# Performance work log

Hardware: AMD Instinct MI355X
Metric: run time of the kernel (lower is better)

## Reference

```python
import jax, jax.numpy as jnp
import numpy as np

B, L, D = 2, 2048, 1024
H = 16
C = 128            # chunk_size
N = L // C         # num chunks
SCALE = float(np.sqrt(D))  # softmax_scale = sqrt(d_model)


def setup_inputs() -> dict:
    key = jax.random.key(0)
    ks = jax.random.split(key, 5)
    return {
        "x": jax.random.normal(ks[0], (B, L, D), dtype=jnp.float32),
        "w_qkv": jax.random.normal(ks[1], (D, 3 * D), dtype=jnp.float32) * (1.0 / np.sqrt(D)),
        "b_qkv": jax.random.normal(ks[2], (3 * D,), dtype=jnp.float32) * 0.02,
        "w_o": jax.random.normal(ks[3], (D, D), dtype=jnp.float32) * (1.0 / np.sqrt(D)),
        "b_o": jax.random.normal(ks[4], (D,), dtype=jnp.float32) * 0.02,
    }


def reference(x, w_qkv, b_qkv, w_o, b_o):
    b, l, d = x.shape
    hd = d // H
    qkv = x @ w_qkv + b_qkv                         # (B,L,3D)
    q, k, v = jnp.split(qkv, 3, axis=-1)
    q = q.reshape(b, l, H, hd)
    k = k.reshape(b, l, H, hd)
    v = v.reshape(b, l, H, hd)

    q_chunks = q.reshape(b, N, C, H, hd)
    k_chunks = k.reshape(b, N, C, H, hd)
    # mean_pool over the chunk dim
    q_pool = q_chunks.mean(axis=2)                  # (B,N,H,hd)
    k_pool = k_chunks.mean(axis=2)

    token2chunk = jnp.einsum('blhd,bnhd->bhln', q, k_pool)          # (B,H,L,N)
    chunk2token = jnp.einsum('bnhd,bnchd->bhnc', q_pool, k_chunks)  # (B,H,N,C)
    # outer product over (n,c) -> full (B,H,L,L) score matrix
    A = token2chunk[..., :, None] * chunk2token[:, :, None, :, :]   # (B,H,L,N,C)
    A = A.reshape(b, H, l, l)

    # direct intra-chunk attention overwrites the diagonal blocks
    direct = jnp.einsum('bnqhd,bnkhd->bhnqk', q_chunks, k_chunks)   # (B,H,N,C,C)
    A6 = A.reshape(b, H, N, C, N, C)
    eye = jnp.eye(N, dtype=bool)[:, None, :, None]                  # (N,1,N,1)
    A6 = jnp.where(eye, direct[:, :, :, :, None, :], A6)
    A = A6.reshape(b, H, l, l)

    # causal mask applied multiplicatively (masked scores become 0, NOT -inf)
    causal = jnp.tril(jnp.ones((l, l), dtype=bool))
    A = jnp.where(causal, A, 0.0) / SCALE
    A = jax.nn.softmax(A, axis=-1)

    out = jnp.einsum('bhqv,bvhd->bhqd', A, v)       # (B,H,L,hd)
    out = out.transpose(0, 2, 1, 3).reshape(b, l, d)
    return out @ w_o + b_o
```

## Files before the change

### kernel.cpp

```cpp
#include <hip/hip_runtime.h>
#include <math.h>

#define B_   2
#define L_   2048
#define D_   1024
#define H_   16
#define HD_  64
#define C_   128
#define N_   16
#define INV_SCALE 0.03125f
#define SCL2 0.0450842200f

typedef _Float16 h8 __attribute__((ext_vector_type(8)));
typedef _Float16 h4 __attribute__((ext_vector_type(4)));
typedef float    f4 __attribute__((ext_vector_type(4)));

#define MFMA16(a, b, c) __builtin_amdgcn_mfma_f32_16x16x32_f16((a), (b), (c), 0, 0, 0)

#if __has_builtin(__builtin_amdgcn_exp2f)
#define EXP2(x) __builtin_amdgcn_exp2f(x)
#else
#define EXP2(x) exp2f(x)
#endif

__device__ __forceinline__ void gl_lds16(const void* g, void* l) {
  __builtin_amdgcn_global_load_lds(
      (const __attribute__((address_space(1))) void*)g,
      (__attribute__((address_space(3))) void*)l, 16, 0, 0);
}

#define SBAR()  do { __builtin_amdgcn_sched_barrier(0); \
                     __builtin_amdgcn_s_barrier();      \
                     __builtin_amdgcn_sched_barrier(0); } while (0)
#define LGKM0() do { asm volatile("s_waitcnt lgkmcnt(0)" ::: "memory"); \
                     __builtin_amdgcn_sched_barrier(0); } while (0)
#define VMW(n)  do { asm volatile("s_waitcnt vmcnt(" #n ")" ::: "memory"); \
                     __builtin_amdgcn_sched_barrier(0); } while (0)

__global__ __launch_bounds__(256) void prep_kernel(
    const float* __restrict__ X, _Float16* __restrict__ Xh,
    const float* __restrict__ Wq, _Float16* __restrict__ WqT,
    const float* __restrict__ Wo, _Float16* __restrict__ WoT)
{
  __shared__ float ts[32][36];
  const int tid = threadIdx.x;
  const int id = blockIdx.x;
  if (id < 4096) {
    int i = id * 1024 + tid * 4;
    float4 v = *(const float4*)(X + i);
    h4 o = { (_Float16)v.x, (_Float16)v.y, (_Float16)v.z, (_Float16)v.w };
    *(h4*)(Xh + i) = o;
    return;
  }
  const float* W; _Float16* WT; int Nc, bx, by;
  if (id < 7168) {
    int idx = id - 4096;
    W = Wq; WT = WqT; Nc = 3072; bx = idx % 96; by = idx / 96;
  } else {
    int idx = id - 7168;
    W = Wo; WT = WoT; Nc = 1024; bx = idx & 31; by = idx >> 5;
  }
  const int n0 = bx * 32, k0 = by * 32;
  {
    int kr = tid >> 3, nc4 = (tid & 7) * 4;
    float4 v = *(const float4*)&W[(size_t)(k0 + kr) * Nc + n0 + nc4];
    ts[kr][nc4+0] = v.x; ts[kr][nc4+1] = v.y; ts[kr][nc4+2] = v.z; ts[kr][nc4+3] = v.w;
  }
  __syncthreads();
  {
    int nr = tid >> 3, kc4 = (tid & 7) * 4;
    h4 o = { (_Float16)ts[kc4+0][nr], (_Float16)ts[kc4+1][nr],
             (_Float16)ts[kc4+2][nr], (_Float16)ts[kc4+3][nr] };
    *(h4*)&WT[(size_t)(n0 + nr) * 1024 + k0 + kc4] = o;
  }
}

__global__ __launch_bounds__(512, 2) void qkv256_kernel(
    const _Float16* __restrict__ A, const _Float16* __restrict__ Bt,
    const float* __restrict__ bias,
    _Float16* __restrict__ Qh, _Float16* __restrict__ Kh, _Float16* __restrict__ VT,
    float* __restrict__ QP, float* __restrict__ KP, float* __restrict__ VCS)
{
  __shared__ __align__(16) _Float16 As[2][16384];
  __shared__ __align__(16) _Float16 Bs[2][12288];

  const int tid = threadIdx.x;
  const int w = tid >> 6, lane = tid & 63;
  const int q = lane >> 4, r = lane & 15, r7 = r & 7;
  const int wm = w >> 2, wn = w & 3;

  const int id = blockIdx.x, xcd = id & 7, slot = id >> 3;
  const int m0 = ((xcd >> 1) * 4 + (slot & 3)) * 256;
  const int n0 = ((xcd & 1) * 8 + (slot >> 2)) * 192;

  const int srow = tid >> 3;
  const int spart = (tid & 7) ^ (srow & 7);
  const _Float16* Asrc = A  + (size_t)(m0 + srow) * 1024 + spart * 8;
  const _Float16* Bsrc = Bt + (size_t)(n0 + srow) * 1024 + spart * 8;
  const int ldst = w * 512;

  const int aoffb = (wm * 128 + r) * 64;
  const int boffb = (wn * 48 + r) * 64;
  const int k0s = (q ^ r7) << 3;
  const int k1s = ((4 + q) ^ r7) << 3;

  auto stA = [&](int cc, int ko, int qq) {
    gl_lds16(Asrc + (size_t)qq * 65536 + ko, &As[cc][qq * 4096 + ldst]);
  };
  auto stB = [&](int cc, int ko, int qq) {
    gl_lds16(Bsrc + (size_t)qq * 65536 + ko, &Bs[cc][qq * 4096 + ldst]);
  };

  f4 acc[8][3];
  #pragma unroll
  for (int m = 0; m < 8; ++m)
    #pragma unroll
    for (int n = 0; n < 3; ++n) acc[m][n] = (f4){0.f, 0.f, 0.f, 0.f};

  stB(0, 0, 0); stB(0, 0, 1); stB(0, 0, 2);
  stA(0, 0, 0); stA(0, 0, 2); stA(0, 0, 1); stA(0, 0, 3);
  VMW(2);
  SBAR();

  for (int t = 0; t < 16; ++t) {
    const int c = t & 1;
    const _Float16* __restrict__ Ab = As[c];
    const _Float16* __restrict__ Bb = Bs[c];
    const int kt = (t + 1) << 6;
    const bool pf = (t < 15);
    h8 af[4], bf[3];

    #pragma unroll
    for (int m = 0; m < 4; ++m) af[m] = *(const h8*)&Ab[aoffb + m * 1024 + k0s];
    #pragma unroll
    for (int n = 0; n < 3; ++n) bf[n] = *(const h8*)&Bb[boffb + n * 1024 + k0s];
    if (pf) { stB(c ^ 1, kt, 0); stB(c ^ 1, kt, 1); }
    SBAR();
    LGKM0();
    __builtin_amdgcn_s_setprio(1);
    #pragma unroll
    for (int m = 0; m < 4; ++m)
      #pragma unroll
      for (int n = 0; n < 3; ++n) acc[m][n] = MFMA16(af[m], bf[n], acc[m][n]);
    __builtin_amdgcn_s_setprio(0);
    __builtin_amdgcn_sched_barrier(0);
    if (pf) { VMW(2); } else { VMW(0); }
    SBAR();

    #pragma unroll
    for (int m = 0; m < 4; ++m) af[m] = *(const h8*)&Ab[aoffb + (4 + m) * 1024 + k0s];
    if (pf) { stB(c ^ 1, kt, 2); stA(c ^ 1, kt, 0); }
    SBAR();
    LGKM0();
    __builtin_amdgcn_s_setprio(1);
    #pragma unroll
    for (int m = 0; m < 4; ++m)
      #pragma unroll
      for (int n = 0; n < 3; ++n) acc[4 + m][n] = MFMA16(af[m], bf[n], acc[4 + m][n]);
    __builtin_amdgcn_s_setprio(0);
    __builtin_amdgcn_sched_barrier(0);
    SBAR();

    #pragma unroll
    for (int m = 0; m < 4; ++m) af[m] = *(const h8*)&Ab[aoffb + m * 1024 + k1s];
    #pragma unroll
    for (int n = 0; n < 3; ++n) bf[n] = *(const h8*)&Bb[boffb + n * 1024 + k1s];
    if (pf) { stA(c ^ 1, kt, 2); stA(c ^ 1, kt, 1); }
    SBAR();
    LGKM0();
    __builtin_amdgcn_s_setprio(1);
    #pragma unroll
    for (int m = 0; m < 4; ++m)
      #pragma unroll
      for (int n = 0; n < 3; ++n) acc[m][n] = MFMA16(af[m], bf[n], acc[m][n]);
    __builtin_amdgcn_s_setprio(0);
    __builtin_amdgcn_sched_barrier(0);
    SBAR();

    #pragma unroll
    for (int m = 0; m < 4; ++m) af[m] = *(const h8*)&Ab[aoffb + (4 + m) * 1024 + k1s];
    if (pf) {
      stA(c ^ 1, kt, 3);
      VMW(2);
    }
    SBAR();
    LGKM0();
    __builtin_amdgcn_s_setprio(1);
    #pragma unroll
    for (int m = 0; m < 4; ++m)
      #pragma unroll
      for (int n = 0; n < 3; ++n) acc[4 + m][n] = MFMA16(af[m], bf[n], acc[4 + m][n]);
    __builtin_amdgcn_s_setprio(0);
    __builtin_amdgcn_sched_barrier(0);
    SBAR();
  }

  const int rb = m0 + wm * 128;
  const int b2 = rb >> 11;
  const int nch = (rb & 2047) >> 7;
  #pragma unroll
  for (int tc = 0; tc < 3; ++tc) {
    const int gn = n0 + wn * 48 + tc * 16 + r;
    const float bj = bias[gn];
    const int which = gn >> 10, rem = gn & 1023;
    const int h2 = rem >> 6, d2 = rem & 63;
    if (which < 2) {
      _Float16* dst = which == 0 ? Qh : Kh;
      #pragma unroll
      for (int m = 0; m < 8; ++m)
        #pragma unroll
        for (int i = 0; i < 4; ++i) {
          const int gm = rb + m * 16 + q * 4 + i;
          const int l2 = gm & 2047;
          dst[(((size_t)(b2 * H_ + h2)) * L_ + l2) * HD_ + d2] =
              (_Float16)(acc[m][tc][i] + bj);
        }
    } else {
      #pragma unroll
      for (int m = 0; m < 8; ++m) {
        const int gm0 = rb + m * 16 + q * 4;
        const int l2 = gm0 & 2047;
        h4 hv = { (_Float16)(acc[m][tc][0] + bj), (_Float16)(acc[m][tc][1] + bj),
                  (_Float16)(acc[m][tc][2] + bj), (_Float16)(acc[m][tc][3] + bj) };
        *(h4*)&VT[((size_t)(b2 * H_ + h2) * HD_ + d2) * L_ + l2] = hv;
      }
    }
    float s2 = 0.f;
    #pragma unroll
    for (int m = 0; m < 8; ++m)
      #pragma unroll
      for (int i = 0; i < 4; ++i) s2 += acc[m][tc][i];
    s2 += __shfl_xor(s2, 16);
    s2 += __shfl_xor(s2, 32);
    if (q == 0) {
      const size_t o = (((size_t)(b2 * H_ + h2)) * N_ + nch) * HD_ + d2;
      if (which == 0)      QP[o] = s2 * (1.f / 128.f) + bj;
      else if (which == 1) KP[o] = s2 * (1.f / 128.f) + bj;
      else                 VCS[o] = s2 + 128.f * bj;
    }
  }
}

template<int MT>
__global__ __launch_bounds__(256, 4) void gemm16_kernel(
    const _Float16* __restrict__ A, const _Float16* __restrict__ Bt,
    const float* __restrict__ bias,
    _Float16* __restrict__ Qh, _Float16* __restrict__ Kh, _Float16* __restrict__ VT,
    float* __restrict__ out,
    float* __restrict__ QP, float* __restrict__ KP, float* __restrict__ VCS,
    int Kd, int mode)
{
  constexpr int SM = MT / 32;
  __shared__ __align__(16) _Float16 As[2][MT * 32];
  __shared__ __align__(16) _Float16 Bs[2][4096];
  __shared__ float cred[2][128];
  const int tid = threadIdx.x;
  const int lane = tid & 63, w = tid >> 6;
  const int q = lane >> 4, r = lane & 15;
  const int mb = (w >> 1) * (MT / 2);
  const int nb = (w & 1) * 64;

  int m0, n0;
  {
    const int id = blockIdx.x;
    const int xcd = id & 7, slot = id >> 3;
    if constexpr (MT == 128) {
      n0 = (xcd * 3 + (slot % 3)) * 128;
      m0 = (slot / 3) * 128;
    } else {
      m0 = (xcd * 8 + (slot >> 3)) * 64;
      n0 = (slot & 7) * 128;
    }
  }

  const int Rr = tid >> 2;
  const int cd = (tid & 3) ^ ((Rr >> 1) & 3);
  const _Float16* Ag = A + (size_t)(m0 + Rr) * Kd + cd * 8;
  const _Float16* Bg = Bt + (size_t)(n0 + Rr) * Kd + cd * 8;
  const size_t rowStep = (size_t)64 * Kd;

  f4 acc[SM][4];
  #pragma unroll
  for (int s = 0; s < SM; ++s)
    #pragma unroll
    for (int t = 0; t < 4; ++t) acc[s][t] = (f4){0.f, 0.f, 0.f, 0.f};

  const int nIter = Kd >> 5;
  const int koff = (q ^ ((r >> 1) & 3)) << 3;

  auto stage = [&](int bf, int kt) {
    _Float16* Asl = &As[bf][w * 512];
    _Float16* Bsl = &Bs[bf][w * 512];
    gl_lds16(Ag + kt, Asl);
    if constexpr (MT == 128) gl_lds16(Ag + kt + rowStep, Asl + 2048);
    gl_lds16(Bg + kt, Bsl);
    gl_lds16(Bg + kt + rowStep, Bsl + 2048);
  };

  stage(0, 0);

  for (int it = 0; it < nIter; ++it) {
    __syncthreads();
    if (it + 1 < nIter) stage((it + 1) & 1, (it + 1) << 5);
    const _Float16* Ab = As[it & 1];
    const _Float16* Bb = Bs[it & 1];
    h8 af[SM], bf4[4];
    #pragma unroll
    for (int s = 0; s < SM; ++s)
      af[s] = *(const h8*)&Ab[(mb + s * 16 + r) * 32 + koff];
    #pragma unroll
    for (int t = 0; t < 4; ++t)
      bf4[t] = *(const h8*)&Bb[(nb + t * 16 + r) * 32 + koff];
    #pragma unroll
    for (int s = 0; s < SM; ++s)
      #pragma unroll
      for (int t = 0; t < 4; ++t)
        acc[s][t] = MFMA16(af[s], bf4[t], acc[s][t]);
  }

  if (mode == 0) {
    #pragma unroll
    for (int t = 0; t < 4; ++t) {
      int gn = n0 + nb + t * 16 + r;
      float bj = bias[gn];
      int which = gn >> 10, rem = gn & 1023;
      int h2 = rem >> 6, d2 = rem & 63;
      if (which < 2) {
        _Float16* dst = which == 0 ? Qh : Kh;
        #pragma unroll
        for (int s = 0; s < SM; ++s)
          #pragma unroll
          for (int i = 0; i < 4; ++i) {
            int gm = m0 + mb + s * 16 + q * 4 + i;
            int b2 = gm >> 11, l2 = gm & 2047;
            dst[(((size_t)(b2 * H_ + h2)) * L_ + l2) * HD_ + d2] =
                (_Float16)(acc[s][t][i] + bj);
          }
      } else {
        #pragma unroll
        for (int s = 0; s < SM; ++s) {
          int gm0 = m0 + mb + s * 16 + q * 4;
          int b2 = gm0 >> 11, l2 = gm0 & 2047;
          h4 hv = { (_Float16)(acc[s][t][0] + bj), (_Float16)(acc[s][t][1] + bj),
                    (_Float16)(acc[s][t][2] + bj), (_Float16)(acc[s][t][3] + bj) };
          *(h4*)&VT[((size_t)(b2 * H_ + h2) * HD_ + d2) * L_ + l2] = hv;
        }
      }
    }
    float colsum[4];
    #pragma unroll
    for (int t = 0; t < 4; ++t) {
      float s2 = 0.f;
      #pragma unroll
      for (int s = 0; s < SM; ++s)
        #pragma unroll
        for (int i = 0; i < 4; ++i) s2 += acc[s][t][i];
      s2 += __shfl_xor(s2, 16);
      s2 += __shfl_xor(s2, 32);
      colsum[t] = s2;
    }
    if (q == 0) {
      #pragma unroll
      for (int t = 0; t < 4; ++t)
        cred[w >> 1][nb + t * 16 + r] = colsum[t];
    }
    __syncthreads();
    if (tid < 128) {
      int jj = tid;
      float ssum = cred[0][jj] + cred[1][jj];
      int gn = n0 + jj;
      float bj = bias[gn];
      int which = gn >> 10, rem = gn & 1023;
      int h2 = rem >> 6, d2 = rem & 63;
      int b2 = m0 >> 11, nch = (m0 & 2047) >> 7;
      size_t o = (((size_t)(b2 * H_ + h2)) * N_ + nch) * HD_ + d2;
      if (which == 0)      QP[o] = ssum * (1.f / 128.f) + bj;
      else if (which == 1) KP[o] = ssum * (1.f / 128.f) + bj;
      else                 VCS[o] = ssum + 128.f * bj;
    }
  } else {
    #pragma unroll
    for (int t = 0; t < 4; ++t) {
      int gn = n0 + nb + t * 16 + r;
      float bj = bias[gn];
      #pragma unroll
      for (int s = 0; s < SM; ++s)
        #pragma unroll
        for (int i = 0; i < 4; ++i) {
          int gm = m0 + mb + s * 16 + q * 4 + i;
          out[(size_t)gm * 1024 + gn] = acc[s][t][i] + bj;
        }
    }
  }
}

__global__ __launch_bounds__(128) void pool2_kernel(
    const float* __restrict__ QP, const _Float16* __restrict__ Kh,
    const float* __restrict__ VCS,
    float* __restrict__ C2T, float* __restrict__ C2TMX, float* __restrict__ C2TMN,
    float* __restrict__ CSUF)
{
  __shared__ float qp_s[64];
  __shared__ float red[4];
  if (blockIdx.x >= 512) {
    int bh = blockIdx.x - 512, d = threadIdx.x;
    if (d < 64) {
      float run = 0.f;
      for (int n = N_ - 1; n >= 0; --n) {
        size_t o = ((size_t)bh * N_ + n) * HD_ + d;
        CSUF[o] = run;
        run += VCS[o];
      }
    }
    return;
  }
  int bh = blockIdx.x >> 4, n = blockIdx.x & 15, tid = threadIdx.x;
  int w = tid >> 6, lane = tid & 63;
  if (tid < 64) qp_s[tid] = QP[((size_t)bh * N_ + n) * HD_ + tid];
  const _Float16* kr = Kh + (((size_t)bh * L_) + n * C_ + tid) * HD_;
  h8 kv[8];
  #pragma unroll
  for (int c8 = 0; c8 < 8; ++c8) kv[c8] = *(const h8*)(kr + c8 * 8);
  __syncthreads();
  float s = 0.f;
  #pragma unroll
  for (int c8 = 0; c8 < 8; ++c8)
    #pragma unroll
    for (int j = 0; j < 8; ++j)
      s = fmaf((float)kv[c8][j], qp_s[c8 * 8 + j], s);
  C2T[((size_t)bh * N_ + n) * C_ + tid] = s;
  float mx = s, mn = s;
  #pragma unroll
  for (int st = 1; st <= 32; st <<= 1) {
    mx = fmaxf(mx, __shfl_xor(mx, st));
    mn = fminf(mn, __shfl_xor(mn, st));
  }
  if (lane == 0) { red[w * 2] = mx; red[w * 2 + 1] = mn; }
  __syncthreads();
  if (tid == 0) {
    C2TMX[bh * N_ + n] = fmaxf(red[0], red[2]);
    C2TMN[bh * N_ + n] = fminf(red[1], red[3]);
  }
}

__global__ __launch_bounds__(512, 4) void attn4_kernel(
    const _Float16* __restrict__ Qh, const _Float16* __restrict__ Kh,
    const _Float16* __restrict__ VT,
    const float* __restrict__ C2T, const float* __restrict__ C2TMX,
    const float* __restrict__ C2TMN, const float* __restrict__ CSUF,
    const float* __restrict__ KP, _Float16* __restrict__ AOh)
{
  __shared__ __align__(16) _Float16 buf0[8192];
  __shared__ __align__(16) _Float16 buf1[8192];
  __shared__ __align__(16) _Float16 buf2[8192];
  __shared__ __align__(16) _Float16 kp_s[1024];
  __shared__ __align__(16) float c2t_s[2][128];

  const int tid = threadIdx.x;
  const int w = tid >> 6, lane = tid & 63;
  const int q = lane >> 4, r = lane & 15;
  const int r7 = r & 7;
  const int id = blockIdx.x;
  const int bh = ((id & 7) << 2) + ((id >> 3) & 3);
  const int nq = 15 - (id >> 5);
  const int l0 = nq * 128;
  const int rowA = l0 + w * 16 + r;
  const int pcw = w * 16 + r;
  const size_t bhL = (size_t)bh * L_;
  const int b2 = bh >> 4, h2 = bh & 15;

  auto stageV = [&](_Float16* buf, int n) {
    #pragma unroll
    for (int j2 = 0; j2 < 2; ++j2) {
      int f = j2 * 512 + tid;
      int d = f >> 4, p = f & 15;
      int c16 = p ^ (d & 7);
      gl_lds16(VT + ((size_t)bh * HD_ + d) * L_ + n * C_ + c16 * 8,
               buf + (size_t)(j2 * 512 + w * 64) * 8);
    }
  };
  auto stageK = [&](_Float16* buf, int n) {
    #pragma unroll
    for (int j2 = 0; j2 < 2; ++j2) {
      int f = j2 * 512 + tid;
      int c = f >> 3, p = f & 7;
      int ck = p ^ (c & 7);
      gl_lds16(Kh + (bhL + n * C_ + c) * HD_ + ck * 8,
               buf + (size_t)(j2 * 512 + w * 64) * 8);
    }
  };
  auto stageC = [&](int bf, int n) {
    if (tid < 32)
      gl_lds16(C2T + ((size_t)bh * N_ + n) * C_ + tid * 4, &c2t_s[bf][0]);
  };

  if (tid < 256) {
    int n4 = tid >> 4, d4 = (tid & 15) * 4;
    float4 kpv = *(const float4*)&KP[((size_t)bh * N_ + n4) * HD_ + d4];
    int sd = ((((d4 >> 3) ^ (n4 & 7)) << 3) | (d4 & 7));
    h4 hv = { (_Float16)kpv.x, (_Float16)kpv.y, (_Float16)kpv.z, (_Float16)kpv.w };
    *(h4*)&kp_s[n4 * 64 + sd] = hv;
  }
  h8 qa0 = *(const h8*)(Qh + (bhL + rowA) * HD_ + q * 8);
  h8 qa1 = *(const h8*)(Qh + (bhL + rowA) * HD_ + 32 + q * 8);
  float mxL = C2TMX[bh * N_ + r];
  float mnL = C2TMN[bh * N_ + r];
  stageK(buf0, nq);
  stageV(buf2, nq);
  if (nq >= 1) stageC(0, nq - 1);
  __syncthreads();

  f4 tvacc = (f4){0.f, 0.f, 0.f, 0.f};
  {
    h8 kpa0 = *(const h8*)&kp_s[r * 64 + ((q ^ r7) << 3)];
    h8 kpa1 = *(const h8*)&kp_s[r * 64 + (((4 + q) ^ r7) << 3)];
    tvacc = MFMA16(kpa0, qa0, tvacc);
    tvacc = MFMA16(kpa1, qa1, tvacc);
  }
  float tvs[4];
  #pragma unroll
  for (int i = 0; i < 4; ++i) tvs[i] = tvacc[i] * SCL2;

  float pm = -1e30f;
  #pragma unroll
  for (int i = 0; i < 4; ++i) {
    int n = q * 4 + i;
    float mx = __shfl(mxL, n);
    float mn = __shfl(mnL, n);
    float cm = fmaxf(tvs[i] * mx, tvs[i] * mn);
    pm = (n < nq) ? fmaxf(pm, cm) : pm;
  }
  pm = fmaxf(pm, __shfl_xor(pm, 16));
  pm = fmaxf(pm, __shfl_xor(pm, 32));

  f4 sc[8];
  #pragma unroll
  for (int u = 0; u < 8; ++u) sc[u] = (f4){0.f, 0.f, 0.f, 0.f};
  {
    h8 kc0 = *(const h8*)&buf0[r * 64 + ((q ^ r7) << 3)];
    h8 kc1 = *(const h8*)&buf0[r * 64 + (((4 + q) ^ r7) << 3)];
    #pragma unroll
    for (int u = 0; u < 8; ++u) {
      h8 kn0, kn1;
      if (u < 7) {
        kn0 = *(const h8*)&buf0[((u + 1) * 16 + r) * 64 + ((q ^ r7) << 3)];
        kn1 = *(const h8*)&buf0[((u + 1) * 16 + r) * 64 + (((4 + q) ^ r7) << 3)];
      }
      sc[u] = MFMA16(kc0, qa0, sc[u]);
      sc[u] = MFMA16(kc1, qa1, sc[u]);
      kc0 = kn0; kc1 = kn1;
    }
  }

  float rm = -1e30f;
  #pragma unroll
  for (int u = 0; u < 8; ++u)
    #pragma unroll
    for (int i = 0; i < 4; ++i) {
      int lcol = u * 16 + q * 4 + i;
      float v = sc[u][i] * SCL2;
      v = (lcol <= pcw) ? v : -1e30f;
      sc[u][i] = v;
      rm = fmaxf(rm, v);
    }
  rm = fmaxf(rm, __shfl_xor(rm, 16));
  rm = fmaxf(rm, __shfl_xor(rm, 32));

  const float M = fmaxf(fmaxf(pm, rm), 0.f);
  const float e0 = EXP2(-M);

  __syncthreads();

  _Float16* pw = (w < 4) ? (buf0 + w * 2048) : (buf1 + (w - 4) * 2048);
  const int pwbase = r * 128 + ((q & 1) << 2);
  float csl = 0.f;
  #pragma unroll
  for (int u = 0; u < 8; ++u) {
    h4 pv4;
    #pragma unroll
    for (int i = 0; i < 4; ++i) {
      float v = sc[u][i];
      float p = (v > -1e29f) ? EXP2(v - M) : 0.f;
      csl += p;
      pv4[i] = (_Float16)p;
    }
    *(h4*)&pw[pwbase + ((((u << 1) | (q >> 1)) ^ r7) << 3)] = pv4;
  }
  csl += __shfl_xor(csl, 16);
  csl += __shfl_xor(csl, 32);
  float den = csl;

  f4 oacc[4], sacc[4];
  #pragma unroll
  for (int t = 0; t < 4; ++t) {
    oacc[t] = (f4){0.f, 0.f, 0.f, 0.f};
    sacc[t] = (f4){0.f, 0.f, 0.f, 0.f};
  }
  {
    h8 pcur = *(const h8*)&pw[r * 128 + ((q ^ r7) << 3)];
    h8 vcur[4];
    #pragma unroll
    for (int t = 0; t < 4; ++t)
      vcur[t] = *(const h8*)&buf2[(t * 16 + r) * 128 + ((q ^ r7) << 3)];
    #pragma unroll
    for (int s = 0; s < 4; ++s) {
      h8 pnxt; h8 vnxt[4];
      if (s < 3) {
        pnxt = *(const h8*)&pw[r * 128 + ((((s + 1) * 4 + q) ^ r7) << 3)];
        #pragma unroll
        for (int t = 0; t < 4; ++t)
          vnxt[t] = *(const h8*)&buf2[(t * 16 + r) * 128 + ((((s + 1) * 4 + q) ^ r7) << 3)];
      }
      h8 mk;
      #pragma unroll
      for (int j2 = 0; j2 < 8; ++j2)
        mk[j2] = (_Float16)((s * 32 + q * 8 + j2 > pcw) ? 1.f : 0.f);
      #pragma unroll
      for (int t = 0; t < 4; ++t) {
        oacc[t] = MFMA16(pcur, vcur[t], oacc[t]);
        sacc[t] = MFMA16(mk, vcur[t], sacc[t]);
      }
      pcur = pnxt;
      #pragma unroll
      for (int t = 0; t < 4; ++t) vcur[t] = vnxt[t];
    }
  }

  __syncthreads();
  if (nq >= 1) stageV(buf1, nq - 1);

  float dsum = 0.f;
  const float negM = -M;
  for (int n = nq - 1; n >= 0; --n) {
    const int k = nq - 1 - n;
    const _Float16* curb = (k & 1) ? buf2 : buf1;
    __syncthreads();
    if (n >= 1) {
      stageV((k & 1) ? buf1 : buf2, n - 1);
      stageC((k + 1) & 1, n - 1);
    }
    int i0 = n & 3;
    float tvx = i0 == 0 ? tvs[0] : i0 == 1 ? tvs[1] : i0 == 2 ? tvs[2] : tvs[3];
    float tvn = __shfl(tvx, ((n >> 2) << 4) + r);
    const float* c2p = c2t_s[k & 1];

    f4 cca = *(const f4*)&c2p[q * 8];
    f4 ccb = *(const f4*)&c2p[q * 8 + 4];
    h8 vcur[4];
    #pragma unroll
    for (int t = 0; t < 4; ++t)
      vcur[t] = *(const h8*)&curb[(t * 16 + r) * 128 + ((q ^ r7) << 3)];

    #pragma unroll
    for (int s = 0; s < 4; ++s) {
      f4 can, cbn; h8 vnxt[4];
      if (s < 3) {
        can = *(const f4*)&c2p[(s + 1) * 32 + q * 8];
        cbn = *(const f4*)&c2p[(s + 1) * 32 + q * 8 + 4];
        #pragma unroll
        for (int t = 0; t < 4; ++t)
          vnxt[t] = *(const h8*)&curb[(t * 16 + r) * 128 + ((((s + 1) * 4 + q) ^ r7) << 3)];
      }
      float p0 = EXP2(fmaf(tvn, cca[0], negM)), p1 = EXP2(fmaf(tvn, cca[1], negM));
      float p2 = EXP2(fmaf(tvn, cca[2], negM)), p3 = EXP2(fmaf(tvn, cca[3], negM));
      float p4 = EXP2(fmaf(tvn, ccb[0], negM)), p5 = EXP2(fmaf(tvn, ccb[1], negM));
      float p6 = EXP2(fmaf(tvn, ccb[2], negM)), p7 = EXP2(fmaf(tvn, ccb[3], negM));
      dsum += p0 + p1 + p2 + p3 + p4 + p5 + p6 + p7;
      h8 pa = { (_Float16)p0, (_Float16)p1, (_Float16)p2, (_Float16)p3,
                (_Float16)p4, (_Float16)p5, (_Float16)p6, (_Float16)p7 };
      #pragma unroll
      for (int t = 0; t < 4; ++t)
        oacc[t] = MFMA16(pa, vcur[t], oacc[t]);
      cca = can; ccb = cbn;
      #pragma unroll
      for (int t = 0; t < 4; ++t) vcur[t] = vnxt[t];
    }
  }
  dsum += __shfl_xor(dsum, 16);
  dsum += __shfl_xor(dsum, 32);
  den += dsum;

  int cnt = (L_ - 1) - rowA;
  den += e0 * (float)cnt;
  float e0r[4], dnr[4];
  #pragma unroll
  for (int i = 0; i < 4; ++i) {
    e0r[i] = __shfl(e0,  (q << 2) + i);
    dnr[i] = __shfl(den, (q << 2) + i);
  }
  #pragma unroll
  for (int t = 0; t < 4; ++t) {
    int d = t * 16 + r;
    float csf = CSUF[((size_t)bh * N_ + nq) * HD_ + d];
    #pragma unroll
    for (int i = 0; i < 4; ++i) {
      int row = l0 + w * 16 + q * 4 + i;
      float suffix = sacc[t][i] + csf;
      float o = (oacc[t][i] + e0r[i] * suffix) / dnr[i];
      AOh[((size_t)b2 * L_ + row) * D_ + h2 * HD_ + d] = (_Float16)o;
    }
  }
}

extern "C" void kernel_launch(void* const* d_in, const int* in_sizes, int n_in,
                              void* d_out, int out_size, void* d_ws, size_t ws_size,
                              hipStream_t stream)
{
  (void)in_sizes; (void)n_in; (void)out_size; (void)ws_size;
  const float* x     = (const float*)d_in[0];
  const float* w_qkv = (const float*)d_in[1];
  const float* b_qkv = (const float*)d_in[2];
  const float* w_o   = (const float*)d_in[3];
  const float* b_o   = (const float*)d_in[4];
  float* out = (float*)d_out;

  char* p = (char*)d_ws;
  _Float16* xh   = (_Float16*)p; p += (size_t)4194304 * 2;
  _Float16* wqT  = (_Float16*)p; p += (size_t)3145728 * 2;
  _Float16* woT  = (_Float16*)p; p += (size_t)1048576 * 2;
  _Float16* Qh   = (_Float16*)p; p += (size_t)4194304 * 2;
  _Float16* Kh   = (_Float16*)p; p += (size_t)4194304 * 2;
  _Float16* VT   = (_Float16*)p; p += (size_t)4194304 * 2;
  _Float16* AOh  = (_Float16*)p; p += (size_t)4194304 * 2;
  float*    C2T  = (float*)p;    p += (size_t)65536 * 4;
  float*    QP   = (float*)p;    p += (size_t)32768 * 4;
  float*    KP   = (float*)p;    p += (size_t)32768 * 4;
  float*    VCS  = (float*)p;    p += (size_t)32768 * 4;
  float*    CSUF = (float*)p;    p += (size_t)32768 * 4;
  float*    MXa  = (float*)p;    p += (size_t)512 * 4;
  float*    MNa  = (float*)p;    p += (size_t)512 * 4;

  prep_kernel<<<8192, 256, 0, stream>>>(x, xh, w_qkv, wqT, w_o, woT);
  qkv256_kernel<<<256, 512, 0, stream>>>(
      xh, wqT, b_qkv, Qh, Kh, VT, QP, KP, VCS);
  pool2_kernel<<<544, 128, 0, stream>>>(QP, Kh, VCS, C2T, MXa, MNa, CSUF);
  attn4_kernel<<<512, 512, 0, stream>>>(
      Qh, Kh, VT, C2T, MXa, MNa, CSUF, KP, AOh);
  gemm16_kernel<64><<<512, 256, 0, stream>>>(
      AOh, woT, b_o, nullptr, nullptr, nullptr, out, nullptr, nullptr, nullptr, D_, 1);
}
```

Before: 171.4 us.

## Process two query chunks per attention block to share V streaming

```diff
diff --git a/kernel.cpp b/kernel.cpp
--- a/kernel.cpp
+++ b/kernel.cpp
@@ -134,7 +134,7 @@
     for (int m = 0; m < 4; ++m) af[m] = *(const h8*)&Ab[aoffb + m * 1024 + k0s];
     #pragma unroll
     for (int n = 0; n < 3; ++n) bf[n] = *(const h8*)&Bb[boffb + n * 1024 + k0s];
-    if (pf) { stB(c ^ 1, kt, 0); stB(c ^ 1, kt, 1); }
+    if (pf) { stB(c ^ 1, kt, 0); stB(c ^ 1, kt, 1); stB(c ^ 1, kt, 2); }
     SBAR();
     LGKM0();
     __builtin_amdgcn_s_setprio(1);
@@ -144,12 +144,12 @@
       for (int n = 0; n < 3; ++n) acc[m][n] = MFMA16(af[m], bf[n], acc[m][n]);
     __builtin_amdgcn_s_setprio(0);
     __builtin_amdgcn_sched_barrier(0);
-    if (pf) { VMW(2); } else { VMW(0); }
+    if (pf) { VMW(3); } else { VMW(0); }
     SBAR();
 
     #pragma unroll
     for (int m = 0; m < 4; ++m) af[m] = *(const h8*)&Ab[aoffb + (4 + m) * 1024 + k0s];
-    if (pf) { stB(c ^ 1, kt, 2); stA(c ^ 1, kt, 0); }
+    if (pf) { stA(c ^ 1, kt, 0); stA(c ^ 1, kt, 2); stA(c ^ 1, kt, 1); }
     SBAR();
     LGKM0();
     __builtin_amdgcn_s_setprio(1);
@@ -165,7 +165,7 @@
     for (int m = 0; m < 4; ++m) af[m] = *(const h8*)&Ab[aoffb + m * 1024 + k1s];
     #pragma unroll
     for (int n = 0; n < 3; ++n) bf[n] = *(const h8*)&Bb[boffb + n * 1024 + k1s];
-    if (pf) { stA(c ^ 1, kt, 2); stA(c ^ 1, kt, 1); }
+    if (pf) { stA(c ^ 1, kt, 3); }
     SBAR();
     LGKM0();
     __builtin_amdgcn_s_setprio(1);
@@ -180,7 +180,6 @@
     #pragma unroll
     for (int m = 0; m < 4; ++m) af[m] = *(const h8*)&Ab[aoffb + (4 + m) * 1024 + k1s];
     if (pf) {
-      stA(c ^ 1, kt, 3);
       VMW(2);
     }
     SBAR();
@@ -244,16 +243,11 @@
 template<int MT>
 __global__ __launch_bounds__(256, 4) void gemm16_kernel(
     const _Float16* __restrict__ A, const _Float16* __restrict__ Bt,
-    const float* __restrict__ bias,
-    _Float16* __restrict__ Qh, _Float16* __restrict__ Kh, _Float16* __restrict__ VT,
-    float* __restrict__ out,
-    float* __restrict__ QP, float* __restrict__ KP, float* __restrict__ VCS,
-    int Kd, int mode)
+    const float* __restrict__ bias, float* __restrict__ out, int Kd)
 {
   constexpr int SM = MT / 32;
   __shared__ __align__(16) _Float16 As[2][MT * 32];
   __shared__ __align__(16) _Float16 Bs[2][4096];
-  __shared__ float cred[2][128];
   const int tid = threadIdx.x;
   const int lane = tid & 63, w = tid >> 6;
   const int q = lane >> 4, r = lane & 15;
@@ -264,13 +258,8 @@
   {
     const int id = blockIdx.x;
     const int xcd = id & 7, slot = id >> 3;
-    if constexpr (MT == 128) {
-      n0 = (xcd * 3 + (slot % 3)) * 128;
-      m0 = (slot / 3) * 128;
-    } else {
-      m0 = (xcd * 8 + (slot >> 3)) * 64;
-      n0 = (slot & 7) * 128;
-    }
+    m0 = (xcd * 8 + (slot >> 3)) * 64;
+    n0 = (slot & 7) * 128;
   }
 
   const int Rr = tid >> 2;
@@ -318,79 +307,17 @@
         acc[s][t] = MFMA16(af[s], bf4[t], acc[s][t]);
   }
 
-  if (mode == 0) {
-    #pragma unroll
-    for (int t = 0; t < 4; ++t) {
-      int gn = n0 + nb + t * 16 + r;
-      float bj = bias[gn];
-      int which = gn >> 10, rem = gn & 1023;
-      int h2 = rem >> 6, d2 = rem & 63;
-      if (which < 2) {
-        _Float16* dst = which == 0 ? Qh : Kh;
-        #pragma unroll
-        for (int s = 0; s < SM; ++s)
-          #pragma unroll
-          for (int i = 0; i < 4; ++i) {
-            int gm = m0 + mb + s * 16 + q * 4 + i;
-            int b2 = gm >> 11, l2 = gm & 2047;
-            dst[(((size_t)(b2 * H_ + h2)) * L_ + l2) * HD_ + d2] =
-                (_Float16)(acc[s][t][i] + bj);
-          }
-      } else {
-        #pragma unroll
-        for (int s = 0; s < SM; ++s) {
-          int gm0 = m0 + mb + s * 16 + q * 4;
-          int b2 = gm0 >> 11, l2 = gm0 & 2047;
-          h4 hv = { (_Float16)(acc[s][t][0] + bj), (_Float16)(acc[s][t][1] + bj),
-                    (_Float16)(acc[s][t][2] + bj), (_Float16)(acc[s][t][3] + bj) };
-          *(h4*)&VT[((size_t)(b2 * H_ + h2) * HD_ + d2) * L_ + l2] = hv;
-        }
+  #pragma unroll
+  for (int t = 0; t < 4; ++t) {
+    int gn = n0 + nb + t * 16 + r;
+    float bj = bias[gn];
+    #pragma unroll
+    for (int s = 0; s < SM; ++s)
+      #pragma unroll
+      for (int i = 0; i < 4; ++i) {
+        int gm = m0 + mb + s * 16 + q * 4 + i;
+        out[(size_t)gm * 1024 + gn] = acc[s][t][i] + bj;
       }
-    }
-    float colsum[4];
-    #pragma unroll
-    for (int t = 0; t < 4; ++t) {
-      float s2 = 0.f;
-      #pragma unroll
-      for (int s = 0; s < SM; ++s)
-        #pragma unroll
-        for (int i = 0; i < 4; ++i) s2 += acc[s][t][i];
-      s2 += __shfl_xor(s2, 16);
-      s2 += __shfl_xor(s2, 32);
-      colsum[t] = s2;
-    }
-    if (q == 0) {
-      #pragma unroll
-      for (int t = 0; t < 4; ++t)
-        cred[w >> 1][nb + t * 16 + r] = colsum[t];
-    }
-    __syncthreads();
-    if (tid < 128) {
-      int jj = tid;
-      float ssum = cred[0][jj] + cred[1][jj];
-      int gn = n0 + jj;
-      float bj = bias[gn];
-      int which = gn >> 10, rem = gn & 1023;
-      int h2 = rem >> 6, d2 = rem & 63;
-      int b2 = m0 >> 11, nch = (m0 & 2047) >> 7;
-      size_t o = (((size_t)(b2 * H_ + h2)) * N_ + nch) * HD_ + d2;
-      if (which == 0)      QP[o] = ssum * (1.f / 128.f) + bj;
-      else if (which == 1) KP[o] = ssum * (1.f / 128.f) + bj;
-      else                 VCS[o] = ssum + 128.f * bj;
-    }
-  } else {
-    #pragma unroll
-    for (int t = 0; t < 4; ++t) {
-      int gn = n0 + nb + t * 16 + r;
-      float bj = bias[gn];
-      #pragma unroll
-      for (int s = 0; s < SM; ++s)
-        #pragma unroll
-        for (int i = 0; i < 4; ++i) {
-          int gm = m0 + mb + s * 16 + q * 4 + i;
-          out[(size_t)gm * 1024 + gn] = acc[s][t][i] + bj;
-        }
-    }
   }
 }
 
@@ -443,16 +370,16 @@
   }
 }
 
-__global__ __launch_bounds__(512, 4) void attn4_kernel(
+__global__ __launch_bounds__(512, 1) void attn5_kernel(
     const _Float16* __restrict__ Qh, const _Float16* __restrict__ Kh,
     const _Float16* __restrict__ VT,
     const float* __restrict__ C2T, const float* __restrict__ C2TMX,
     const float* __restrict__ C2TMN, const float* __restrict__ CSUF,
     const float* __restrict__ KP, _Float16* __restrict__ AOh)
 {
-  __shared__ __align__(16) _Float16 buf0[8192];
-  __shared__ __align__(16) _Float16 buf1[8192];
-  __shared__ __align__(16) _Float16 buf2[8192];
+  __shared__ __align__(16) _Float16 kb[16384];
+  __shared__ __align__(16) _Float16 pwb[16384];
+  __shared__ __align__(16) _Float16 vbuf[2][8192];
   __shared__ __align__(16) _Float16 kp_s[1024];
   __shared__ __align__(16) float c2t_s[2][128];
 
@@ -462,9 +389,10 @@
   const int r7 = r & 7;
   const int id = blockIdx.x;
   const int bh = ((id & 7) << 2) + ((id >> 3) & 3);
-  const int nq = 15 - (id >> 5);
-  const int l0 = nq * 128;
-  const int rowA = l0 + w * 16 + r;
+  const int gg = 7 - (id >> 5);
+  const int c0 = gg * 2, c1 = c0 + 1;
+  const int rA = c0 * 128 + w * 16 + r;
+  const int rB = c1 * 128 + w * 16 + r;
   const int pcw = w * 16 + r;
   const size_t bhL = (size_t)bh * L_;
   const int b2 = bh >> 4, h2 = bh & 15;
@@ -501,58 +429,68 @@
     h4 hv = { (_Float16)kpv.x, (_Float16)kpv.y, (_Float16)kpv.z, (_Float16)kpv.w };
     *(h4*)&kp_s[n4 * 64 + sd] = hv;
   }
-  h8 qa0 = *(const h8*)(Qh + (bhL + rowA) * HD_ + q * 8);
-  h8 qa1 = *(const h8*)(Qh + (bhL + rowA) * HD_ + 32 + q * 8);
+  h8 qa0 = *(const h8*)(Qh + (bhL + rA) * HD_ + q * 8);
+  h8 qa1 = *(const h8*)(Qh + (bhL + rA) * HD_ + 32 + q * 8);
+  h8 qb0 = *(const h8*)(Qh + (bhL + rB) * HD_ + q * 8);
+  h8 qb1 = *(const h8*)(Qh + (bhL + rB) * HD_ + 32 + q * 8);
   float mxL = C2TMX[bh * N_ + r];
   float mnL = C2TMN[bh * N_ + r];
-  stageK(buf0, nq);
-  stageV(buf2, nq);
-  if (nq >= 1) stageC(0, nq - 1);
+  stageK(kb, c0);
+  stageK(kb + 8192, c1);
+  stageV(vbuf[0], c0);
+  stageV(vbuf[1], c1);
+  stageC(0, c0);
   __syncthreads();
 
-  f4 tvacc = (f4){0.f, 0.f, 0.f, 0.f};
+  f4 tva = (f4){0.f, 0.f, 0.f, 0.f};
+  f4 tvb = (f4){0.f, 0.f, 0.f, 0.f};
   {
     h8 kpa0 = *(const h8*)&kp_s[r * 64 + ((q ^ r7) << 3)];
     h8 kpa1 = *(const h8*)&kp_s[r * 64 + (((4 + q) ^ r7) << 3)];
-    tvacc = MFMA16(kpa0, qa0, tvacc);
-    tvacc = MFMA16(kpa1, qa1, tvacc);
-  }
-  float tvs[4];
-  #pragma unroll
-  for (int i = 0; i < 4; ++i) tvs[i] = tvacc[i] * SCL2;
-
-  float pm = -1e30f;
+    tva = MFMA16(kpa0, qa0, tva);
+    tva = MFMA16(kpa1, qa1, tva);
+    tvb = MFMA16(kpa0, qb0, tvb);
+    tvb = MFMA16(kpa1, qb1, tvb);
+  }
+  float tvs0[4], tvs1[4];
+  #pragma unroll
+  for (int i = 0; i < 4; ++i) { tvs0[i] = tva[i] * SCL2; tvs1[i] = tvb[i] * SCL2; }
+
+  float pm0 = -1e30f, pm1 = -1e30f;
   #pragma unroll
   for (int i = 0; i < 4; ++i) {
     int n = q * 4 + i;
     float mx = __shfl(mxL, n);
     float mn = __shfl(mnL, n);
-    float cm = fmaxf(tvs[i] * mx, tvs[i] * mn);
-    pm = (n < nq) ? fmaxf(pm, cm) : pm;
-  }
-  pm = fmaxf(pm, __shfl_xor(pm, 16));
-  pm = fmaxf(pm, __shfl_xor(pm, 32));
+    float cm0 = fmaxf(tvs0[i] * mx, tvs0[i] * mn);
+    float cm1 = fmaxf(tvs1[i] * mx, tvs1[i] * mn);
+    pm0 = (n < c0) ? fmaxf(pm0, cm0) : pm0;
+    pm1 = (n < c1) ? fmaxf(pm1, cm1) : pm1;
+  }
+  pm0 = fmaxf(pm0, __shfl_xor(pm0, 16));
+  pm0 = fmaxf(pm0, __shfl_xor(pm0, 32));
+  pm1 = fmaxf(pm1, __shfl_xor(pm1, 16));
+  pm1 = fmaxf(pm1, __shfl_xor(pm1, 32));
 
   f4 sc[8];
   #pragma unroll
   for (int u = 0; u < 8; ++u) sc[u] = (f4){0.f, 0.f, 0.f, 0.f};
   {
-    h8 kc0 = *(const h8*)&buf0[r * 64 + ((q ^ r7) << 3)];
-    h8 kc1 = *(const h8*)&buf0[r * 64 + (((4 + q) ^ r7) << 3)];
+    h8 kc0 = *(const h8*)&kb[r * 64 + ((q ^ r7) << 3)];
+    h8 kc1 = *(const h8*)&kb[r * 64 + (((4 + q) ^ r7) << 3)];
     #pragma unroll
     for (int u = 0; u < 8; ++u) {
       h8 kn0, kn1;
       if (u < 7) {
-        kn0 = *(const h8*)&buf0[((u + 1) * 16 + r) * 64 + ((q ^ r7) << 3)];
-        kn1 = *(const h8*)&buf0[((u + 1) * 16 + r) * 64 + (((4 + q) ^ r7) << 3)];
+        kn0 = *(const h8*)&kb[((u + 1) * 16 + r) * 64 + ((q ^ r7) << 3)];
+        kn1 = *(const h8*)&kb[((u + 1) * 16 + r) * 64 + (((4 + q) ^ r7) << 3)];
       }
       sc[u] = MFMA16(kc0, qa0, sc[u]);
       sc[u] = MFMA16(kc1, qa1, sc[u]);
       kc0 = kn0; kc1 = kn1;
     }
   }
-
-  float rm = -1e30f;
+  float rm0 = -1e30f;
   #pragma unroll
   for (int u = 0; u < 8; ++u)
     #pragma unroll
@@ -561,143 +499,215 @@
       float v = sc[u][i] * SCL2;
       v = (lcol <= pcw) ? v : -1e30f;
       sc[u][i] = v;
-      rm = fmaxf(rm, v);
-    }
-  rm = fmaxf(rm, __shfl_xor(rm, 16));
-  rm = fmaxf(rm, __shfl_xor(rm, 32));
-
-  const float M = fmaxf(fmaxf(pm, rm), 0.f);
-  const float e0 = EXP2(-M);
-
-  __syncthreads();
-
-  _Float16* pw = (w < 4) ? (buf0 + w * 2048) : (buf1 + (w - 4) * 2048);
+      rm0 = fmaxf(rm0, v);
+    }
+  rm0 = fmaxf(rm0, __shfl_xor(rm0, 16));
+  rm0 = fmaxf(rm0, __shfl_xor(rm0, 32));
+  const float M0 = fmaxf(fmaxf(pm0, rm0), 0.f);
+  const float e00 = EXP2(-M0);
+
+  _Float16* pw0 = pwb + w * 2048;
   const int pwbase = r * 128 + ((q & 1) << 2);
-  float csl = 0.f;
+  float csl0 = 0.f;
   #pragma unroll
   for (int u = 0; u < 8; ++u) {
     h4 pv4;
     #pragma unroll
     for (int i = 0; i < 4; ++i) {
       float v = sc[u][i];
-      float p = (v > -1e29f) ? EXP2(v - M) : 0.f;
-      csl += p;
+      float p = (v > -1e29f) ? EXP2(v - M0) : 0.f;
+      csl0 += p;
       pv4[i] = (_Float16)p;
     }
-    *(h4*)&pw[pwbase + ((((u << 1) | (q >> 1)) ^ r7) << 3)] = pv4;
-  }
-  csl += __shfl_xor(csl, 16);
-  csl += __shfl_xor(csl, 32);
-  float den = csl;
-
-  f4 oacc[4], sacc[4];
+    *(h4*)&pw0[pwbase + ((((u << 1) | (q >> 1)) ^ r7) << 3)] = pv4;
+  }
+  csl0 += __shfl_xor(csl0, 16);
+  csl0 += __shfl_xor(csl0, 32);
+
+  #pragma unroll
+  for (int u = 0; u < 8; ++u) sc[u] = (f4){0.f, 0.f, 0.f, 0.f};
+  {
+    h8 kc0 = *(const h8*)&kb[8192 + r * 64 + ((q ^ r7) << 3)];
+    h8 kc1 = *(const h8*)&kb[8192 + r * 64 + (((4 + q) ^ r7) << 3)];
+    #pragma unroll
+    for (int u = 0; u < 8; ++u) {
+      h8 kn0, kn1;
+      if (u < 7) {
+        kn0 = *(const h8*)&kb[8192 + ((u + 1) * 16 + r) * 64 + ((q ^ r7) << 3)];
+        kn1 = *(const h8*)&kb[8192 + ((u + 1) * 16 + r) * 64 + (((4 + q) ^ r7) << 3)];
+      }
+      sc[u] = MFMA16(kc0, qb0, sc[u]);
+      sc[u] = MFMA16(kc1, qb1, sc[u]);
+      kc0 = kn0; kc1 = kn1;
+    }
+  }
+  float rm1 = -1e30f;
+  #pragma unroll
+  for (int u = 0; u < 8; ++u)
+    #pragma unroll
+    for (int i = 0; i < 4; ++i) {
+      int lcol = u * 16 + q * 4 + i;
+      float v = sc[u][i] * SCL2;
+      v = (lcol <= pcw) ? v : -1e30f;
+      sc[u][i] = v;
+      rm1 = fmaxf(rm1, v);
+    }
+  rm1 = fmaxf(rm1, __shfl_xor(rm1, 16));
+  rm1 = fmaxf(rm1, __shfl_xor(rm1, 32));
+  const float M1 = fmaxf(fmaxf(pm1, rm1), 0.f);
+  const float e01 = EXP2(-M1);
+
+  __syncthreads();
+
+  _Float16* pw1 = kb + w * 2048;
+  float csl1 = 0.f;
+  #pragma unroll
+  for (int u = 0; u < 8; ++u) {
+    h4 pv4;
+    #pragma unroll
+    for (int i = 0; i < 4; ++i) {
+      float v = sc[u][i];
+      float p = (v > -1e29f) ? EXP2(v - M1) : 0.f;
+      csl1 += p;
+      pv4[i] = (_Float16)p;
+    }
+    *(h4*)&pw1[pwbase + ((((u << 1) | (q >> 1)) ^ r7) << 3)] = pv4;
+  }
+  csl1 += __shfl_xor(csl1, 16);
+  csl1 += __shfl_xor(csl1, 32);
+
+  f4 oacc0[4], sacc0[4], oacc1[4], sacc1[4];
   #pragma unroll
   for (int t = 0; t < 4; ++t) {
-    oacc[t] = (f4){0.f, 0.f, 0.f, 0.f};
-    sacc[t] = (f4){0.f, 0.f, 0.f, 0.f};
-  }
+    oacc0[t] = (f4){0.f, 0.f, 0.f, 0.f};
+    sacc0[t] = (f4){0.f, 0.f, 0.f, 0.f};
+    oacc1[t] = (f4){0.f, 0.f, 0.f, 0.f};
+    sacc1[t] = (f4){0.f, 0.f, 0.f, 0.f};
+  }
+  float dsum0 = 0.f, dsum1 = 0.f;
+  const float nM0 = -M0, nM1 = -M1;
   {
-    h8 pcur = *(const h8*)&pw[r * 128 + ((q ^ r7) << 3)];
-    h8 vcur[4];
-    #pragma unroll
-    for (int t = 0; t < 4; ++t)
-      vcur[t] = *(const h8*)&buf2[(t * 16 + r) * 128 + ((q ^ r7) << 3)];
+    int i0 = c0 & 3;
+    float tvx = i0 == 0 ? tvs1[0] : i0 == 1 ? tvs1[1] : i0 == 2 ? tvs1[2] : tvs1[3];
+    float tvA = __shfl(tvx, ((c0 >> 2) << 4) + r);
     #pragma unroll
     for (int s = 0; s < 4; ++s) {
-      h8 pnxt; h8 vnxt[4];
-      if (s < 3) {
-        pnxt = *(const h8*)&pw[r * 128 + ((((s + 1) * 4 + q) ^ r7) << 3)];
-        #pragma unroll
-        for (int t = 0; t < 4; ++t)
-          vnxt[t] = *(const h8*)&buf2[(t * 16 + r) * 128 + ((((s + 1) * 4 + q) ^ r7) << 3)];
-      }
+      h8 vcur[4];
+      #pragma unroll
+      for (int t = 0; t < 4; ++t)
+        vcur[t] = *(const h8*)&vbuf[0][(t * 16 + r) * 128 + (((s * 4 + q) ^ r7) << 3)];
+      h8 pa0 = *(const h8*)&pw0[r * 128 + (((s * 4 + q) ^ r7) << 3)];
+      const float* cp = &c2t_s[0][s * 32 + q * 8];
+      float p0 = EXP2(fmaf(tvA, cp[0], nM1)), p1 = EXP2(fmaf(tvA, cp[1], nM1));
+      float p2 = EXP2(fmaf(tvA, cp[2], nM1)), p3 = EXP2(fmaf(tvA, cp[3], nM1));
+      float p4 = EXP2(fmaf(tvA, cp[4], nM1)), p5 = EXP2(fmaf(tvA, cp[5], nM1));
+      float p6 = EXP2(fmaf(tvA, cp[6], nM1)), p7 = EXP2(fmaf(tvA, cp[7], nM1));
+      dsum1 += p0 + p1 + p2 + p3 + p4 + p5 + p6 + p7;
+      h8 par = { (_Float16)p0, (_Float16)p1, (_Float16)p2, (_Float16)p3,
+                 (_Float16)p4, (_Float16)p5, (_Float16)p6, (_Float16)p7 };
       h8 mk;
       #pragma unroll
       for (int j2 = 0; j2 < 8; ++j2)
         mk[j2] = (_Float16)((s * 32 + q * 8 + j2 > pcw) ? 1.f : 0.f);
       #pragma unroll
       for (int t = 0; t < 4; ++t) {
-        oacc[t] = MFMA16(pcur, vcur[t], oacc[t]);
-        sacc[t] = MFMA16(mk, vcur[t], sacc[t]);
+        oacc0[t] = MFMA16(pa0, vcur[t], oacc0[t]);
+        sacc0[t] = MFMA16(mk, vcur[t], sacc0[t]);
+        oacc1[t] = MFMA16(par, vcur[t], oacc1[t]);
       }
-      pcur = pnxt;
-      #pragma unroll
-      for (int t = 0; t < 4; ++t) vcur[t] = vnxt[t];
     }
   }
 
   __syncthreads();
-  if (nq >= 1) stageV(buf1, nq - 1);
-
-  float dsum = 0.f;
-  const float negM = -M;
-  for (int n = nq - 1; n >= 0; --n) {
-    const int k = nq - 1 - n;
-    const _Float16* curb = (k & 1) ? buf2 : buf1;
+  if (c0 >= 1) { stageV(vbuf[0], c0 - 1); stageC(1, c0 - 1); }
+
+  #pragma unroll
+  for (int s = 0; s < 4; ++s) {
+    h8 vcur[4];
+    #pragma unroll
+    for (int t = 0; t < 4; ++t)
+      vcur[t] = *(const h8*)&vbuf[1][(t * 16 + r) * 128 + (((s * 4 + q) ^ r7) << 3)];
+    h8 pa1 = *(const h8*)&pw1[r * 128 + (((s * 4 + q) ^ r7) << 3)];
+    h8 mk;
+    #pragma unroll
+    for (int j2 = 0; j2 < 8; ++j2)
+      mk[j2] = (_Float16)((s * 32 + q * 8 + j2 > pcw) ? 1.f : 0.f);
+    #pragma unroll
+    for (int t = 0; t < 4; ++t) {
+      oacc1[t] = MFMA16(pa1, vcur[t], oacc1[t]);
+      sacc1[t] = MFMA16(mk, vcur[t], sacc1[t]);
+    }
+  }
+
+  for (int n = c0 - 1; n >= 0; --n) {
+    const int k = c0 - 1 - n;
+    const _Float16* curb = vbuf[k & 1];
     __syncthreads();
-    if (n >= 1) {
-      stageV((k & 1) ? buf1 : buf2, n - 1);
-      stageC((k + 1) & 1, n - 1);
-    }
+    if (n >= 1) { stageV(vbuf[(k + 1) & 1], n - 1); stageC(k & 1, n - 1); }
+    const float* c2p = c2t_s[(k + 1) & 1];
     int i0 = n & 3;
-    float tvx = i0 == 0 ? tvs[0] : i0 == 1 ? tvs[1] : i0 == 2 ? tvs[2] : tvs[3];
-    float tvn = __shfl(tvx, ((n >> 2) << 4) + r);
-    const float* c2p = c2t_s[k & 1];
-
-    f4 cca = *(const f4*)&c2p[q * 8];
-    f4 ccb = *(const f4*)&c2p[q * 8 + 4];
-    h8 vcur[4];
-    #pragma unroll
-    for (int t = 0; t < 4; ++t)
-      vcur[t] = *(const h8*)&curb[(t * 16 + r) * 128 + ((q ^ r7) << 3)];
-
+    float tvx0 = i0 == 0 ? tvs0[0] : i0 == 1 ? tvs0[1] : i0 == 2 ? tvs0[2] : tvs0[3];
+    float tvx1 = i0 == 0 ? tvs1[0] : i0 == 1 ? tvs1[1] : i0 == 2 ? tvs1[2] : tvs1[3];
+    float tvn0 = __shfl(tvx0, ((n >> 2) << 4) + r);
+    float tvn1 = __shfl(tvx1, ((n >> 2) << 4) + r);
     #pragma unroll
     for (int s = 0; s < 4; ++s) {
-      f4 can, cbn; h8 vnxt[4];
-      if (s < 3) {
-        can = *(const f4*)&c2p[(s + 1) * 32 + q * 8];
-        cbn = *(const f4*)&c2p[(s + 1) * 32 + q * 8 + 4];
-        #pragma unroll
-        for (int t = 0; t < 4; ++t)
-          vnxt[t] = *(const h8*)&curb[(t * 16 + r) * 128 + ((((s + 1) * 4 + q) ^ r7) << 3)];
+      h8 vcur[4];
+      #pragma unroll
+      for (int t = 0; t < 4; ++t)
+        vcur[t] = *(const h8*)&curb[(t * 16 + r) * 128 + (((s * 4 + q) ^ r7) << 3)];
+      const float* cp = &c2p[s * 32 + q * 8];
+      float c0v = cp[0], c1v = cp[1], c2v = cp[2], c3v = cp[3];
+      float c4v = cp[4], c5v = cp[5], c6v = cp[6], c7v = cp[7];
+      float a0 = EXP2(fmaf(tvn0, c0v, nM0)), a1 = EXP2(fmaf(tvn0, c1v, nM0));
+      float a2 = EXP2(fmaf(tvn0, c2v, nM0)), a3 = EXP2(fmaf(tvn0, c3v, nM0));
+      float a4 = EXP2(fmaf(tvn0, c4v, nM0)), a5 = EXP2(fmaf(tvn0, c5v, nM0));
+      float a6 = EXP2(fmaf(tvn0, c6v, nM0)), a7 = EXP2(fmaf(tvn0, c7v, nM0));
+      float b0 = EXP2(fmaf(tvn1, c0v, nM1)), b1 = EXP2(fmaf(tvn1, c1v, nM1));
+      float b2v = EXP2(fmaf(tvn1, c2v, nM1)), b3 = EXP2(fmaf(tvn1, c3v, nM1));
+      float b4 = EXP2(fmaf(tvn1, c4v, nM1)), b5 = EXP2(fmaf(tvn1, c5v, nM1));
+      float b6 = EXP2(fmaf(tvn1, c6v, nM1)), b7 = EXP2(fmaf(tvn1, c7v, nM1));
+      dsum0 += a0 + a1 + a2 + a3 + a4 + a5 + a6 + a7;
+      dsum1 += b0 + b1 + b2v + b3 + b4 + b5 + b6 + b7;
+      h8 paA = { (_Float16)a0, (_Float16)a1, (_Float16)a2, (_Float16)a3,
+                 (_Float16)a4, (_Float16)a5, (_Float16)a6, (_Float16)a7 };
+      h8 paB = { (_Float16)b0, (_Float16)b1, (_Float16)b2v, (_Float16)b3,
+                 (_Float16)b4, (_Float16)b5, (_Float16)b6, (_Float16)b7 };
+      #pragma unroll
+      for (int t = 0; t < 4; ++t) {
+        oacc0[t] = MFMA16(paA, vcur[t], oacc0[t]);
+        oacc1[t] = MFMA16(paB, vcur[t], oacc1[t]);
       }
-      float p0 = EXP2(fmaf(tvn, cca[0], negM)), p1 = EXP2(fmaf(tvn, cca[1], negM));
-      float p2 = EXP2(fmaf(tvn, cca[2], negM)), p3 = EXP2(fmaf(tvn, cca[3], negM));
-      float p4 = EXP2(fmaf(tvn, ccb[0], negM)), p5 = EXP2(fmaf(tvn, ccb[1], negM));
-      float p6 = EXP2(fmaf(tvn, ccb[2], negM)), p7 = EXP2(fmaf(tvn, ccb[3], negM));
-      dsum += p0 + p1 + p2 + p3 + p4 + p5 + p6 + p7;
-      h8 pa = { (_Float16)p0, (_Float16)p1, (_Float16)p2, (_Float16)p3,
-                (_Float16)p4, (_Float16)p5, (_Float16)p6, (_Float16)p7 };
-      #pragma unroll
-      for (int t = 0; t < 4; ++t)
-        oacc[t] = MFMA16(pa, vcur[t], oacc[t]);
-      cca = can; ccb = cbn;
-      #pragma unroll
-      for (int t = 0; t < 4; ++t) vcur[t] = vnxt[t];
-    }
-  }
-  dsum += __shfl_xor(dsum, 16);
-  dsum += __shfl_xor(dsum, 32);
-  den += dsum;
-
-  int cnt = (L_ - 1) - rowA;
-  den += e0 * (float)cnt;
-  float e0r[4], dnr[4];
+    }
+  }
+  dsum0 += __shfl_xor(dsum0, 16);
+  dsum0 += __shfl_xor(dsum0, 32);
+  dsum1 += __shfl_xor(dsum1, 16);
+  dsum1 += __shfl_xor(dsum1, 32);
+
+  float den0 = csl0 + dsum0 + e00 * (float)((L_ - 1) - rA);
+  float den1 = csl1 + dsum1 + e01 * (float)((L_ - 1) - rB);
+  float e0r0[4], dnr0[4], e0r1[4], dnr1[4];
   #pragma unroll
   for (int i = 0; i < 4; ++i) {
-    e0r[i] = __shfl(e0,  (q << 2) + i);
-    dnr[i] = __shfl(den, (q << 2) + i);
+    e0r0[i] = __shfl(e00,  (q << 2) + i);
+    dnr0[i] = __shfl(den0, (q << 2) + i);
+    e0r1[i] = __shfl(e01,  (q << 2) + i);
+    dnr1[i] = __shfl(den1, (q << 2) + i);
   }
   #pragma unroll
   for (int t = 0; t < 4; ++t) {
     int d = t * 16 + r;
-    float csf = CSUF[((size_t)bh * N_ + nq) * HD_ + d];
+    float csf0 = CSUF[((size_t)bh * N_ + c0) * HD_ + d];
+    float csf1 = CSUF[((size_t)bh * N_ + c1) * HD_ + d];
     #pragma unroll
     for (int i = 0; i < 4; ++i) {
-      int row = l0 + w * 16 + q * 4 + i;
-      float suffix = sacc[t][i] + csf;
-      float o = (oacc[t][i] + e0r[i] * suffix) / dnr[i];
-      AOh[((size_t)b2 * L_ + row) * D_ + h2 * HD_ + d] = (_Float16)o;
+      int row0 = c0 * 128 + w * 16 + q * 4 + i;
+      int row1 = c1 * 128 + w * 16 + q * 4 + i;
+      float o0 = (oacc0[t][i] + e0r0[i] * (sacc0[t][i] + csf0)) / dnr0[i];
+      float o1 = (oacc1[t][i] + e0r1[i] * (sacc1[t][i] + csf1)) / dnr1[i];
+      AOh[((size_t)b2 * L_ + row0) * D_ + h2 * HD_ + d] = (_Float16)o0;
+      AOh[((size_t)b2 * L_ + row1) * D_ + h2 * HD_ + d] = (_Float16)o1;
     }
   }
 }
@@ -734,8 +744,8 @@
   qkv256_kernel<<<256, 512, 0, stream>>>(
       xh, wqT, b_qkv, Qh, Kh, VT, QP, KP, VCS);
   pool2_kernel<<<544, 128, 0, stream>>>(QP, Kh, VCS, C2T, MXa, MNa, CSUF);
-  attn4_kernel<<<512, 512, 0, stream>>>(
+  attn5_kernel<<<256, 512, 0, stream>>>(
       Qh, Kh, VT, C2T, MXa, MNa, CSUF, KP, AOh);
   gemm16_kernel<64><<<512, 256, 0, stream>>>(
-      AOh, woT, b_o, nullptr, nullptr, nullptr, out, nullptr, nullptr, nullptr, D_, 1);
+      AOh, woT, b_o, out, D_);
 }
```

After: 177.3 us. 1.03x slower.
